# Kernel tuning notes

Hardware: AMD Instinct MI355X
Metric: run time of the kernel (lower is better)

The kernel has to match this reference:

```python
import jax, jax.numpy as jnp
import numpy as np

B, N, C, H, W_, K, POS = 1, 100000, 128, 256, 256, 4, 36


def setup_inputs() -> dict:
    key = jax.random.key(0)
    ks = jax.random.split(key, 12)
    inp = {}
    # query coords in [-1, 1] (grid_sample normalized space)
    inp["query"] = jax.random.uniform(ks[0], (B, N, 3), jnp.float32, -1.0, 1.0)
    inp["pe"] = jax.random.normal(ks[1], (B, N, POS), jnp.float32)
    for i, p in enumerate(["xy", "xz", "yz"]):
        inp[f"feat_{p}"] = jax.random.normal(ks[2 + i], (B, C, H, W_), jnp.float32)
        inp[f"Wa_{p}"] = jax.random.normal(ks[5 + i], (POS, K), jnp.float32) * 0.1
        inp[f"ba_{p}"] = jnp.zeros((K,), jnp.float32)
        # offsets initialized to zero in the module; use small random so sampling is non-trivial
        inp[f"Wo_{p}"] = jax.random.normal(ks[8 + i], (POS, 2 * K), jnp.float32) * 0.02
        inp[f"bo_{p}"] = jnp.zeros((2 * K,), jnp.float32)
    return inp


def _bilinear_border(feat, gx, gy):
    """F.grid_sample(feat, grid, align_corners=False, padding_mode='border').
    feat: [B,C,H,W]; gx,gy: [B,N,K] normalized x (width) and y (height) coords.
    Returns [B,C,N,K]."""
    b, c, h, w = feat.shape
    # unnormalize (align_corners=False) then border-clip
    x = jnp.clip(((gx + 1.0) * w - 1.0) * 0.5, 0.0, w - 1.0)
    y = jnp.clip(((gy + 1.0) * h - 1.0) * 0.5, 0.0, h - 1.0)
    x0 = jnp.floor(x)
    y0 = jnp.floor(y)
    wx = x - x0  # [B,N,K]
    wy = y - y0
    xi0 = x0.astype(jnp.int32)
    yi0 = y0.astype(jnp.int32)
    xi1 = jnp.minimum(xi0 + 1, w - 1)
    yi1 = jnp.minimum(yi0 + 1, h - 1)
    ff = feat.reshape(b, c, h * w)
    gather = jax.vmap(lambda f, lin: f[:, lin])  # [C,HW],[N,K] -> [C,N,K]
    v00 = gather(ff, yi0 * w + xi0)
    v01 = gather(ff, yi0 * w + xi1)
    v10 = gather(ff, yi1 * w + xi0)
    v11 = gather(ff, yi1 * w + xi1)
    wx_ = wx[:, None]
    wy_ = wy[:, None]
    return (v00 * (1.0 - wx_) * (1.0 - wy_) + v01 * wx_ * (1.0 - wy_)
            + v10 * (1.0 - wx_) * wy_ + v11 * wx_ * wy_)


def _sample_plane(coords, pe, feat, Wa, ba, Wo, bo):
    b, n, _ = coords.shape
    attn = jax.nn.softmax(pe @ Wa + ba, axis=-1)            # [B,N,K]
    off = (pe @ Wo + bo).reshape(b, n, K, 2)                 # [B,N,K,2]
    sc = coords[:, :, None, :] + off                         # [B,N,K,2]
    # torch code flips last dim before grid_sample: grid x = sc[...,1], y = sc[...,0]
    sampled = _bilinear_border(feat, sc[..., 1], sc[..., 0])  # [B,C,N,K]
    out = jnp.einsum('bcnk,bnk->bnc', sampled, attn)         # weighted sum over K
    return out


def reference(query, pe, feat_xy, feat_xz, feat_yz,
              Wa_xy, ba_xy, Wo_xy, bo_xy,
              Wa_xz, ba_xz, Wo_xz, bo_xz,
              Wa_yz, ba_yz, Wo_yz, bo_yz):
    idx_xy = jnp.array([0, 1])
    idx_xz = jnp.array([0, 2])
    idx_yz = jnp.array([1, 2])
    f_xy = _sample_plane(query[..., idx_xy], pe, feat_xy, Wa_xy, ba_xy, Wo_xy, bo_xy)
    f_xz = _sample_plane(query[..., idx_xz], pe, feat_xz, Wa_xz, ba_xz, Wo_xz, bo_xz)
    f_yz = _sample_plane(query[..., idx_yz], pe, feat_yz, Wa_yz, ba_yz, Wo_yz, bo_yz)
    return f_xy + f_xz + f_yz
```

## Files before the change

kernel.cpp:

```cpp
#include <hip/hip_runtime.h>
#include <hip/hip_fp16.h>
#include <math.h>

#define NQ   100000
#define CCH  128
#define HDIM 256
#define WDIM 256
#define HW   (HDIM * WDIM)
#define KPTS 4
#define PDIM 36
#define NBIN 4096
#define RECW 100

__device__ inline int axis_bin(float x) {
  int b = (int)((x + 1.0f) * 8.0f);
  return min(15, max(0, b));
}
__device__ inline unsigned int spread4(unsigned int x) {
  return (x & 1u) | ((x & 2u) << 2) | ((x & 4u) << 4) | ((x & 8u) << 6);
}
__device__ inline unsigned int bin_of(float x, float y, float z) {
  return spread4((unsigned int)axis_bin(x)) |
         (spread4((unsigned int)axis_bin(y)) << 1) |
         (spread4((unsigned int)axis_bin(z)) << 2);
}

__global__ void transpose_kernel(const float* __restrict__ f0,
                                 const float* __restrict__ f1,
                                 const float* __restrict__ f2,
                                 __half2* __restrict__ out) {
  __shared__ float tile[64][65];
  const int plane = blockIdx.z;
  const float* __restrict__ f = (plane == 0) ? f0 : ((plane == 1) ? f1 : f2);
  __half2* __restrict__ o = out + (size_t)plane * (size_t)HW * (CCH / 2);
  const int hw0 = blockIdx.x * 64;
  const int c0 = blockIdx.y * 64;
  const int t = threadIdx.x;
  const int c_l = t >> 6;
  const int hw_l = t & 63;
#pragma unroll
  for (int i = 0; i < 16; ++i) {
    tile[c_l + 4 * i][hw_l] = f[(size_t)(c0 + c_l + 4 * i) * HW + (hw0 + hw_l)];
  }
  __syncthreads();
#pragma unroll
  for (int i = 0; i < 8; ++i) {
    const int idx = t + 256 * i;
    const int j = idx & 31;
    const int r = idx >> 5;
    o[(size_t)(hw0 + r) * (CCH / 2) + (c0 / 2 + j)] =
        __floats2half2_rn(tile[2 * j][r], tile[2 * j + 1][r]);
  }
}

__global__ void zero_kernel(unsigned int* __restrict__ counts) {
  const int t = blockIdx.x * 256 + threadIdx.x;
  if (t < NBIN) counts[t] = 0;
}

__global__ void hist_kernel(const float* __restrict__ query,
                            unsigned int* __restrict__ counts) {
  const int q = blockIdx.x * 256 + threadIdx.x;
  if (q >= NQ) return;
  const unsigned int b = bin_of(query[q * 3 + 0], query[q * 3 + 1], query[q * 3 + 2]);
  atomicAdd(&counts[b], 1u);
}

__global__ void scan_kernel(const unsigned int* __restrict__ counts,
                            unsigned int* __restrict__ offs) {
  __shared__ unsigned int s[1024];
  const int t = threadIdx.x;
  const unsigned int c0 = counts[4 * t + 0];
  const unsigned int c1 = counts[4 * t + 1];
  const unsigned int c2 = counts[4 * t + 2];
  const unsigned int c3 = counts[4 * t + 3];
  const unsigned int sum = c0 + c1 + c2 + c3;
  s[t] = sum;
  __syncthreads();
  for (int d = 1; d < 1024; d <<= 1) {
    const unsigned int v = (t >= d) ? s[t - d] : 0u;
    __syncthreads();
    s[t] += v;
    __syncthreads();
  }
  const unsigned int base = s[t] - sum;
  offs[4 * t + 0] = base;
  offs[4 * t + 1] = base + c0;
  offs[4 * t + 2] = base + c0 + c1;
  offs[4 * t + 3] = base + c0 + c1 + c2;
}

__global__ void scatter_kernel(const float* __restrict__ query,
                               unsigned int* __restrict__ offs,
                               unsigned int* __restrict__ perm) {
  const int q = blockIdx.x * 256 + threadIdx.x;
  if (q >= NQ) return;
  const unsigned int b = bin_of(query[q * 3 + 0], query[q * 3 + 1], query[q * 3 + 2]);
  const unsigned int pos = atomicAdd(&offs[b], 1u);
  perm[pos] = (unsigned int)q;
}

__global__ void weights_kernel(const float* __restrict__ query,
                               const float* __restrict__ pe,
                               const unsigned int* __restrict__ perm,
                               const float* __restrict__ Wa0, const float* __restrict__ ba0,
                               const float* __restrict__ Wo0, const float* __restrict__ bo0,
                               const float* __restrict__ Wa1, const float* __restrict__ ba1,
                               const float* __restrict__ Wo1, const float* __restrict__ bo1,
                               const float* __restrict__ Wa2, const float* __restrict__ ba2,
                               const float* __restrict__ Wo2, const float* __restrict__ bo2,
                               float* __restrict__ rec) {
  __shared__ float sWa[3][PDIM][4];
  __shared__ float sWo[3][PDIM][8];
  __shared__ float sba[3][4];
  __shared__ float sbo[3][8];
  const int t = threadIdx.x;
  {
    float* wa = &sWa[0][0][0];
    for (int i = t; i < 144; i += 256) { wa[i] = Wa0[i]; wa[144 + i] = Wa1[i]; wa[288 + i] = Wa2[i]; }
    float* wo = &sWo[0][0][0];
    for (int i = t; i < 288; i += 256) { wo[i] = Wo0[i]; wo[288 + i] = Wo1[i]; wo[576 + i] = Wo2[i]; }
    if (t < 4) { sba[0][t] = ba0[t]; sba[1][t] = ba1[t]; sba[2][t] = ba2[t]; }
    if (t < 8) { sbo[0][t] = bo0[t]; sbo[1][t] = bo1[t]; sbo[2][t] = bo2[t]; }
  }
  __syncthreads();

  const int n = blockIdx.x * 256 + t;
  if (n >= NQ) return;
  const int q = (int)perm[n];

  float p[PDIM];
  const float4* pe4 = (const float4*)(pe + (size_t)q * PDIM);
#pragma unroll
  for (int i = 0; i < 9; ++i) {
    float4 v = pe4[i];
    p[4 * i + 0] = v.x; p[4 * i + 1] = v.y; p[4 * i + 2] = v.z; p[4 * i + 3] = v.w;
  }

  float la[3][4], of[3][8];
#pragma unroll
  for (int pl = 0; pl < 3; ++pl) {
#pragma unroll
    for (int k = 0; k < 4; ++k) la[pl][k] = sba[pl][k];
#pragma unroll
    for (int d = 0; d < 8; ++d) of[pl][d] = sbo[pl][d];
  }
#pragma unroll 4
  for (int j = 0; j < PDIM; ++j) {
    const float pj = p[j];
#pragma unroll
    for (int pl = 0; pl < 3; ++pl) {
#pragma unroll
      for (int k = 0; k < 4; ++k) la[pl][k] = fmaf(pj, sWa[pl][j][k], la[pl][k]);
#pragma unroll
      for (int d = 0; d < 8; ++d) of[pl][d] = fmaf(pj, sWo[pl][j][d], of[pl][d]);
    }
  }

  const float qx = query[q * 3 + 0];
  const float qy = query[q * 3 + 1];
  const float qz = query[q * 3 + 2];

  float* r = rec + (size_t)n * RECW;
  r[0] = __uint_as_float((unsigned int)q);
  r[1] = 0.0f; r[2] = 0.0f; r[3] = 0.0f;

#pragma unroll
  for (int pl = 0; pl < 3; ++pl) {
    const float m = fmaxf(fmaxf(la[pl][0], la[pl][1]), fmaxf(la[pl][2], la[pl][3]));
    const float e0 = expf(la[pl][0] - m);
    const float e1 = expf(la[pl][1] - m);
    const float e2 = expf(la[pl][2] - m);
    const float e3 = expf(la[pl][3] - m);
    const float inv = 1.0f / (e0 + e1 + e2 + e3);
    float at[4] = {e0 * inv, e1 * inv, e2 * inv, e3 * inv};

    const float ca = (pl == 2) ? qy : qx;
    const float cb = (pl == 0) ? qy : qz;
    const unsigned int pbase = (unsigned int)pl * (unsigned int)HW * (CCH / 2);
#pragma unroll
    for (int k = 0; k < KPTS; ++k) {
      const float gy = ca + of[pl][k * 2 + 0];
      const float gx = cb + of[pl][k * 2 + 1];
      float x = ((gx + 1.0f) * (float)WDIM - 1.0f) * 0.5f;
      float y = ((gy + 1.0f) * (float)HDIM - 1.0f) * 0.5f;
      x = fminf(fmaxf(x, 0.0f), (float)(WDIM - 1));
      y = fminf(fmaxf(y, 0.0f), (float)(HDIM - 1));
      const float x0f = floorf(x), y0f = floorf(y);
      const float wx = x - x0f, wy = y - y0f;
      const int xi0 = (int)x0f, yi0 = (int)y0f;
      const int xi1 = min(xi0 + 1, WDIM - 1);
      const int yi1 = min(yi0 + 1, HDIM - 1);
      const float a = at[k];
      float* g = r + 4 + 8 * (pl * 4 + k);
      g[0] = a * (1.0f - wx) * (1.0f - wy);
      g[1] = a * wx * (1.0f - wy);
      g[2] = a * (1.0f - wx) * wy;
      g[3] = a * wx * wy;
      g[4] = __uint_as_float(pbase + (unsigned int)(yi0 * WDIM + xi0) * (CCH / 2));
      g[5] = __uint_as_float(pbase + (unsigned int)(yi0 * WDIM + xi1) * (CCH / 2));
      g[6] = __uint_as_float(pbase + (unsigned int)(yi1 * WDIM + xi0) * (CCH / 2));
      g[7] = __uint_as_float(pbase + (unsigned int)(yi1 * WDIM + xi1) * (CCH / 2));
    }
  }
}

__global__ void sample_kernel(const float* __restrict__ rec,
                              const __half2* __restrict__ featT,
                              float* __restrict__ out) {
  const int lane = threadIdx.x & 63;
  const int wid = threadIdx.x >> 6;
  const int b = blockIdx.x;
  const int sb = (b & 7) * 3125 + (b >> 3);
  int i = sb * 4 + wid;
  i = __builtin_amdgcn_readfirstlane(i);

  const float* __restrict__ r = rec + (size_t)i * RECW;
  const int q = (int)__float_as_uint(r[0]);
  const __half2* __restrict__ fl = featT + lane;

  float accx = 0.0f, accy = 0.0f;
#pragma unroll
  for (int j = 0; j < 12; ++j) {
    const float w00 = r[4 + 8 * j + 0];
    const float w01 = r[4 + 8 * j + 1];
    const float w10 = r[4 + 8 * j + 2];
    const float w11 = r[4 + 8 * j + 3];
    const unsigned int a00 = __float_as_uint(r[4 + 8 * j + 4]);
    const unsigned int a01 = __float_as_uint(r[4 + 8 * j + 5]);
    const unsigned int a10 = __float_as_uint(r[4 + 8 * j + 6]);
    const unsigned int a11 = __float_as_uint(r[4 + 8 * j + 7]);
    const __half2 v00 = fl[a00];
    const __half2 v01 = fl[a01];
    const __half2 v10 = fl[a10];
    const __half2 v11 = fl[a11];
    accx = fmaf(w00, __low2float(v00), accx);
    accy = fmaf(w00, __high2float(v00), accy);
    accx = fmaf(w01, __low2float(v01), accx);
    accy = fmaf(w01, __high2float(v01), accy);
    accx = fmaf(w10, __low2float(v10), accx);
    accy = fmaf(w10, __high2float(v10), accy);
    accx = fmaf(w11, __low2float(v11), accx);
    accy = fmaf(w11, __high2float(v11), accy);
  }
  *(float2*)(out + (size_t)q * CCH + lane * 2) = make_float2(accx, accy);
}

__global__ void fused_fallback(const float* __restrict__ query,
                               const float* __restrict__ pe,
                               const float* __restrict__ f0,
                               const float* __restrict__ f1,
                               const float* __restrict__ f2,
                               const float* __restrict__ Wa0, const float* __restrict__ ba0,
                               const float* __restrict__ Wo0, const float* __restrict__ bo0,
                               const float* __restrict__ Wa1, const float* __restrict__ ba1,
                               const float* __restrict__ Wo1, const float* __restrict__ bo1,
                               const float* __restrict__ Wa2, const float* __restrict__ ba2,
                               const float* __restrict__ Wo2, const float* __restrict__ bo2,
                               float* __restrict__ out) {
  const int lane = threadIdx.x & 63;
  const int wid = threadIdx.x >> 6;
  int q = blockIdx.x * 4 + wid;
  q = __builtin_amdgcn_readfirstlane(q);
  if (q >= NQ) return;
  const float qx = query[q * 3 + 0];
  const float qy = query[q * 3 + 1];
  const float qz = query[q * 3 + 2];
  const float* pep = pe + (size_t)q * PDIM;
  const int c0i = lane * 2, c1i = lane * 2 + 1;
  float accx = 0.0f, accy = 0.0f;
#pragma unroll
  for (int pl = 0; pl < 3; ++pl) {
    const float* Wa = (pl == 0) ? Wa0 : ((pl == 1) ? Wa1 : Wa2);
    const float* ba = (pl == 0) ? ba0 : ((pl == 1) ? ba1 : ba2);
    const float* Wo = (pl == 0) ? Wo0 : ((pl == 1) ? Wo1 : Wo2);
    const float* bo = (pl == 0) ? bo0 : ((pl == 1) ? bo1 : bo2);
    const float* f = (pl == 0) ? f0 : ((pl == 1) ? f1 : f2);
    float la[4] = {ba[0], ba[1], ba[2], ba[3]};
    float of[8];
    for (int d = 0; d < 8; ++d) of[d] = bo[d];
    for (int j = 0; j < PDIM; ++j) {
      const float pj = pep[j];
      for (int k = 0; k < 4; ++k) la[k] = fmaf(pj, Wa[j * 4 + k], la[k]);
      for (int d = 0; d < 8; ++d) of[d] = fmaf(pj, Wo[j * 8 + d], of[d]);
    }
    const float m = fmaxf(fmaxf(la[0], la[1]), fmaxf(la[2], la[3]));
    float e[4], s = 0.0f;
    for (int k = 0; k < 4; ++k) { e[k] = expf(la[k] - m); s += e[k]; }
    const float inv = 1.0f / s;
    const float ca = (pl == 2) ? qy : qx;
    const float cb = (pl == 0) ? qy : qz;
    for (int k = 0; k < 4; ++k) {
      const float gy = ca + of[k * 2 + 0];
      const float gx = cb + of[k * 2 + 1];
      float x = ((gx + 1.0f) * (float)WDIM - 1.0f) * 0.5f;
      float y = ((gy + 1.0f) * (float)HDIM - 1.0f) * 0.5f;
      x = fminf(fmaxf(x, 0.0f), (float)(WDIM - 1));
      y = fminf(fmaxf(y, 0.0f), (float)(HDIM - 1));
      const float x0f = floorf(x), y0f = floorf(y);
      const float wx = x - x0f, wy = y - y0f;
      const int xi0 = (int)x0f, yi0 = (int)y0f;
      const int xi1 = min(xi0 + 1, WDIM - 1);
      const int yi1 = min(yi0 + 1, HDIM - 1);
      const float a = e[k] * inv;
      const float w00 = a * (1.0f - wx) * (1.0f - wy);
      const float w01 = a * wx * (1.0f - wy);
      const float w10 = a * (1.0f - wx) * wy;
      const float w11 = a * wx * wy;
      const size_t p00 = (size_t)(yi0 * WDIM + xi0);
      const size_t p01 = (size_t)(yi0 * WDIM + xi1);
      const size_t p10 = (size_t)(yi1 * WDIM + xi0);
      const size_t p11 = (size_t)(yi1 * WDIM + xi1);
      const float* fa = f + (size_t)c0i * HW;
      const float* fb = f + (size_t)c1i * HW;
      accx += w00 * fa[p00] + w01 * fa[p01] + w10 * fa[p10] + w11 * fa[p11];
      accy += w00 * fb[p00] + w01 * fb[p01] + w10 * fb[p10] + w11 * fb[p11];
    }
  }
  *(float2*)(out + (size_t)q * CCH + lane * 2) = make_float2(accx, accy);
}

extern "C" void kernel_launch(void* const* d_in, const int* in_sizes, int n_in,
                              void* d_out, int out_size, void* d_ws, size_t ws_size,
                              hipStream_t stream) {
  const float* query = (const float*)d_in[0];
  const float* pe    = (const float*)d_in[1];
  const float* feat0 = (const float*)d_in[2];
  const float* Wa0   = (const float*)d_in[3];
  const float* ba0   = (const float*)d_in[4];
  const float* Wo0   = (const float*)d_in[5];
  const float* bo0   = (const float*)d_in[6];
  const float* feat1 = (const float*)d_in[7];
  const float* Wa1   = (const float*)d_in[8];
  const float* ba1   = (const float*)d_in[9];
  const float* Wo1   = (const float*)d_in[10];
  const float* bo1   = (const float*)d_in[11];
  const float* feat2 = (const float*)d_in[12];
  const float* Wa2   = (const float*)d_in[13];
  const float* ba2   = (const float*)d_in[14];
  const float* Wo2   = (const float*)d_in[15];
  const float* bo2   = (const float*)d_in[16];
  float* out = (float*)d_out;

  const size_t featT_elems = 3ull * HW * (CCH / 2);
  const size_t need = featT_elems * 4 + (size_t)NQ * RECW * 4 +
                      (size_t)NBIN * 8 + (size_t)NQ * 4;

  if (ws_size >= need) {
    __half2* featT = (__half2*)d_ws;
    float* rec = (float*)(featT + featT_elems);
    unsigned int* counts = (unsigned int*)(rec + (size_t)NQ * RECW);
    unsigned int* offs = counts + NBIN;
    unsigned int* perm = offs + NBIN;

    zero_kernel<<<dim3((NBIN + 255) / 256), dim3(256), 0, stream>>>(counts);
    transpose_kernel<<<dim3(HW / 64, CCH / 64, 3), dim3(256), 0, stream>>>(
        feat0, feat1, feat2, featT);
    hist_kernel<<<dim3((NQ + 255) / 256), dim3(256), 0, stream>>>(query, counts);
    scan_kernel<<<dim3(1), dim3(1024), 0, stream>>>(counts, offs);
    scatter_kernel<<<dim3((NQ + 255) / 256), dim3(256), 0, stream>>>(query, offs, perm);
    weights_kernel<<<dim3((NQ + 255) / 256), dim3(256), 0, stream>>>(
        query, pe, perm, Wa0, ba0, Wo0, bo0, Wa1, ba1, Wo1, bo1,
        Wa2, ba2, Wo2, bo2, rec);
    sample_kernel<<<dim3(NQ / 4), dim3(256), 0, stream>>>(rec, featT, out);
  } else {
    fused_fallback<<<dim3((NQ + 3) / 4), dim3(256), 0, stream>>>(
        query, pe, feat0, feat1, feat2,
        Wa0, ba0, Wo0, bo0, Wa1, ba1, Wo1, bo1, Wa2, ba2, Wo2, bo2, out);
  }
}
```

Measured before the change: 157.8 us.

## Compress per-query sample records and refine Morton binning for query sorting

Each query's sample record shrinks from 100 to 40 words. The four corner addresses are now one base address plus two neighbour flag bits, and the bilinear weights are stored as packed fp16 pairs. This cuts the traffic that writes and reads the intermediate records. The Morton sort grid goes from 16^3 to 32^3 bins for finer spatial locality of gathers, and the scan is widened to match. The zero kernel is replaced with hipMemsetAsync. Storing weights in fp16 adds rounding error on top of the fp16 features.

```diff
diff --git a/kernel.cpp b/kernel.cpp
--- a/kernel.cpp
+++ b/kernel.cpp
@@ -9,20 +9,20 @@
 #define HW   (HDIM * WDIM)
 #define KPTS 4
 #define PDIM 36
-#define NBIN 4096
-#define RECW 100
+#define NBIN 32768
+#define RECW 40
 
 __device__ inline int axis_bin(float x) {
-  int b = (int)((x + 1.0f) * 8.0f);
-  return min(15, max(0, b));
-}
-__device__ inline unsigned int spread4(unsigned int x) {
-  return (x & 1u) | ((x & 2u) << 2) | ((x & 4u) << 4) | ((x & 8u) << 6);
+  int b = (int)((x + 1.0f) * 16.0f);
+  return min(31, max(0, b));
+}
+__device__ inline unsigned int spread5(unsigned int x) {
+  return (x & 1u) | ((x & 2u) << 2) | ((x & 4u) << 4) | ((x & 8u) << 6) | ((x & 16u) << 8);
 }
 __device__ inline unsigned int bin_of(float x, float y, float z) {
-  return spread4((unsigned int)axis_bin(x)) |
-         (spread4((unsigned int)axis_bin(y)) << 1) |
-         (spread4((unsigned int)axis_bin(z)) << 2);
+  return spread5((unsigned int)axis_bin(x)) |
+         (spread5((unsigned int)axis_bin(y)) << 1) |
+         (spread5((unsigned int)axis_bin(z)) << 2);
 }
 
 __global__ void transpose_kernel(const float* __restrict__ f0,
@@ -53,11 +53,6 @@
   }
 }
 
-__global__ void zero_kernel(unsigned int* __restrict__ counts) {
-  const int t = blockIdx.x * 256 + threadIdx.x;
-  if (t < NBIN) counts[t] = 0;
-}
-
 __global__ void hist_kernel(const float* __restrict__ query,
                             unsigned int* __restrict__ counts) {
   const int q = blockIdx.x * 256 + threadIdx.x;
@@ -70,11 +65,11 @@
                             unsigned int* __restrict__ offs) {
   __shared__ unsigned int s[1024];
   const int t = threadIdx.x;
-  const unsigned int c0 = counts[4 * t + 0];
-  const unsigned int c1 = counts[4 * t + 1];
-  const unsigned int c2 = counts[4 * t + 2];
-  const unsigned int c3 = counts[4 * t + 3];
-  const unsigned int sum = c0 + c1 + c2 + c3;
+  unsigned int c[32];
+  unsigned int sum = 0;
+  const int base_i = t * 32;
+#pragma unroll
+  for (int j = 0; j < 32; ++j) { c[j] = counts[base_i + j]; sum += c[j]; }
   s[t] = sum;
   __syncthreads();
   for (int d = 1; d < 1024; d <<= 1) {
@@ -83,11 +78,9 @@
     s[t] += v;
     __syncthreads();
   }
-  const unsigned int base = s[t] - sum;
-  offs[4 * t + 0] = base;
-  offs[4 * t + 1] = base + c0;
-  offs[4 * t + 2] = base + c0 + c1;
-  offs[4 * t + 3] = base + c0 + c1 + c2;
+  unsigned int run = s[t] - sum;
+#pragma unroll
+  for (int j = 0; j < 32; ++j) { offs[base_i + j] = run; run += c[j]; }
 }
 
 __global__ void scatter_kernel(const float* __restrict__ query,
@@ -109,7 +102,7 @@
                                const float* __restrict__ Wo1, const float* __restrict__ bo1,
                                const float* __restrict__ Wa2, const float* __restrict__ ba2,
                                const float* __restrict__ Wo2, const float* __restrict__ bo2,
-                               float* __restrict__ rec) {
+                               unsigned int* __restrict__ rec) {
   __shared__ float sWa[3][PDIM][4];
   __shared__ float sWo[3][PDIM][8];
   __shared__ float sba[3][4];
@@ -161,9 +154,8 @@
   const float qy = query[q * 3 + 1];
   const float qz = query[q * 3 + 2];
 
-  float* r = rec + (size_t)n * RECW;
-  r[0] = __uint_as_float((unsigned int)q);
-  r[1] = 0.0f; r[2] = 0.0f; r[3] = 0.0f;
+  unsigned int* r = rec + (size_t)n * RECW;
+  r[0] = (unsigned int)q;
 
 #pragma unroll
   for (int pl = 0; pl < 3; ++pl) {
@@ -189,23 +181,26 @@
       const float x0f = floorf(x), y0f = floorf(y);
       const float wx = x - x0f, wy = y - y0f;
       const int xi0 = (int)x0f, yi0 = (int)y0f;
-      const int xi1 = min(xi0 + 1, WDIM - 1);
-      const int yi1 = min(yi0 + 1, HDIM - 1);
+      const unsigned int dx = (xi0 + 1 <= WDIM - 1) ? 1u : 0u;
+      const unsigned int dy = (yi0 + 1 <= HDIM - 1) ? 1u : 0u;
       const float a = at[k];
-      float* g = r + 4 + 8 * (pl * 4 + k);
-      g[0] = a * (1.0f - wx) * (1.0f - wy);
-      g[1] = a * wx * (1.0f - wy);
-      g[2] = a * (1.0f - wx) * wy;
-      g[3] = a * wx * wy;
-      g[4] = __uint_as_float(pbase + (unsigned int)(yi0 * WDIM + xi0) * (CCH / 2));
-      g[5] = __uint_as_float(pbase + (unsigned int)(yi0 * WDIM + xi1) * (CCH / 2));
-      g[6] = __uint_as_float(pbase + (unsigned int)(yi1 * WDIM + xi0) * (CCH / 2));
-      g[7] = __uint_as_float(pbase + (unsigned int)(yi1 * WDIM + xi1) * (CCH / 2));
+      const float w00 = a * (1.0f - wx) * (1.0f - wy);
+      const float w01 = a * wx * (1.0f - wy);
+      const float w10 = a * (1.0f - wx) * wy;
+      const float w11 = a * wx * wy;
+      const unsigned int a00 = pbase + (unsigned int)(yi0 * WDIM + xi0) * (CCH / 2);
+      const int j = pl * 4 + k;
+      r[1 + 3 * j] = a00 | (dx << 24) | (dy << 25);
+      const __half2 h01 = __floats2half2_rn(w00, w01);
+      const __half2 h23 = __floats2half2_rn(w10, w11);
+      r[2 + 3 * j] = *(const unsigned int*)&h01;
+      r[3 + 3 * j] = *(const unsigned int*)&h23;
     }
   }
-}
-
-__global__ void sample_kernel(const float* __restrict__ rec,
+  r[37] = 0u; r[38] = 0u; r[39] = 0u;
+}
+
+__global__ void sample_kernel(const unsigned int* __restrict__ rec,
                               const __half2* __restrict__ featT,
                               float* __restrict__ out) {
   const int lane = threadIdx.x & 63;
@@ -215,21 +210,28 @@
   int i = sb * 4 + wid;
   i = __builtin_amdgcn_readfirstlane(i);
 
-  const float* __restrict__ r = rec + (size_t)i * RECW;
-  const int q = (int)__float_as_uint(r[0]);
+  const unsigned int* __restrict__ r = rec + (size_t)i * RECW;
+  const int q = (int)r[0];
   const __half2* __restrict__ fl = featT + lane;
 
   float accx = 0.0f, accy = 0.0f;
 #pragma unroll
   for (int j = 0; j < 12; ++j) {
-    const float w00 = r[4 + 8 * j + 0];
-    const float w01 = r[4 + 8 * j + 1];
-    const float w10 = r[4 + 8 * j + 2];
-    const float w11 = r[4 + 8 * j + 3];
-    const unsigned int a00 = __float_as_uint(r[4 + 8 * j + 4]);
-    const unsigned int a01 = __float_as_uint(r[4 + 8 * j + 5]);
-    const unsigned int a10 = __float_as_uint(r[4 + 8 * j + 6]);
-    const unsigned int a11 = __float_as_uint(r[4 + 8 * j + 7]);
+    const unsigned int pk = r[1 + 3 * j];
+    const unsigned int w01u = r[2 + 3 * j];
+    const unsigned int w23u = r[3 + 3 * j];
+    const unsigned int a00 = pk & 0xFFFFFFu;
+    const unsigned int xo = (pk >> 18) & 64u;
+    const unsigned int yo = (pk >> 11) & 16384u;
+    const unsigned int a01 = a00 + xo;
+    const unsigned int a10 = a00 + yo;
+    const unsigned int a11 = a01 + yo;
+    const __half2 h01 = __builtin_bit_cast(__half2, w01u);
+    const __half2 h23 = __builtin_bit_cast(__half2, w23u);
+    const float w00 = __low2float(h01);
+    const float w01 = __high2float(h01);
+    const float w10 = __low2float(h23);
+    const float w11 = __high2float(h23);
     const __half2 v00 = fl[a00];
     const __half2 v01 = fl[a01];
     const __half2 v10 = fl[a10];
@@ -348,12 +350,12 @@
 
   if (ws_size >= need) {
     __half2* featT = (__half2*)d_ws;
-    float* rec = (float*)(featT + featT_elems);
-    unsigned int* counts = (unsigned int*)(rec + (size_t)NQ * RECW);
+    unsigned int* rec = (unsigned int*)(d_ws) + featT_elems;
+    unsigned int* counts = rec + (size_t)NQ * RECW;
     unsigned int* offs = counts + NBIN;
     unsigned int* perm = offs + NBIN;
 
-    zero_kernel<<<dim3((NBIN + 255) / 256), dim3(256), 0, stream>>>(counts);
+    hipMemsetAsync(counts, 0, NBIN * sizeof(unsigned int), stream);
     transpose_kernel<<<dim3(HW / 64, CCH / 64, 3), dim3(256), 0, stream>>>(
         feat0, feat1, feat2, featT);
     hist_kernel<<<dim3((NQ + 255) / 256), dim3(256), 0, stream>>>(query, counts);
```

New measurement: 151.1 us. 4.3% less time.
